# Kernel tuning notes

Hardware: AMD Instinct MI355X
Metric: run time of the kernel (lower is better)

## Reference

```python
import jax, jax.numpy as jnp
import numpy as np

B, T, F, H = 256, 4096, 16, 64

def setup_inputs() -> dict:
    key = jax.random.key(0)
    ks = jax.random.split(key, 16)
    rn = lambda k, s, sc=0.1: jax.random.normal(k, s, dtype=jnp.float32) * sc
    return {
        'x':    rn(ks[0], (B, T, F), 1.0),
        'Wi1':  rn(ks[1], (F, 3 * H)), 'bi1': jnp.zeros((3 * H,), jnp.float32),
        'Whr1': rn(ks[2], (H, H)), 'Whz1': rn(ks[3], (H, H)), 'Whn1': rn(ks[4], (H, H)),
        'bhn1': jnp.zeros((H,), jnp.float32),
        'Wi2':  rn(ks[5], (H, 3 * H)), 'bi2': jnp.zeros((3 * H,), jnp.float32),
        'Whr2': rn(ks[6], (H, H)), 'Whz2': rn(ks[7], (H, H)), 'Whn2': rn(ks[8], (H, H)),
        'bhn2': jnp.zeros((H,), jnp.float32),
        'Wp':   rn(ks[9], (F, H)), 'bp': jnp.zeros((H,), jnp.float32),
        'Wa':   rn(ks[10], (H, 1)), 'ba': jnp.zeros((1,), jnp.float32),
        'W1':   rn(ks[11], (H, 128)), 'b1': jnp.zeros((128,), jnp.float32),
        'W2':   rn(ks[12], (128, 64)), 'b2': jnp.zeros((64,), jnp.float32),
        'W3':   rn(ks[13], (64, 32)), 'b3': jnp.zeros((32,), jnp.float32),
        'W4':   rn(ks[14], (32, 2)), 'b4': jnp.zeros((2,), jnp.float32),
    }

def gru_layer(x, Wi, bi, Whr, Whz, Whn, bhn):
    # flax GRUCell math: r/z hidden kernels bias-free; n hidden kernel has bias.
    b, h = x.shape[0], Whr.shape[0]
    xi = jnp.einsum('btf,fk->btk', x, Wi) + bi  # precompute input projections (B,T,3H)
    def step(hprev, xt):
        ir, iz, inn = jnp.split(xt, 3, axis=-1)
        r = jax.nn.sigmoid(ir + hprev @ Whr)
        z = jax.nn.sigmoid(iz + hprev @ Whz)
        n = jnp.tanh(inn + r * (hprev @ Whn + bhn))
        hnew = (1.0 - z) * n + z * hprev
        return hnew, hnew
    h0 = jnp.zeros((b, h), x.dtype)
    _, ys = jax.lax.scan(step, h0, jnp.swapaxes(xi, 0, 1))  # (T,B,H)
    return jnp.swapaxes(ys, 0, 1)  # (B,T,H)

def reference(x, Wi1, bi1, Whr1, Whz1, Whn1, bhn1,
              Wi2, bi2, Whr2, Whz2, Whn2, bhn2,
              Wp, bp, Wa, ba, W1, b1, W2, b2, W3, b3, W4, b4):
    o1 = gru_layer(x, Wi1, bi1, Whr1, Whz1, Whn1, bhn1)
    x_proj = jnp.einsum('btf,fh->bth', x, Wp) + bp  # F != H -> project
    o1 = o1 + 0.5 * x_proj
    o2 = gru_layer(o1, Wi2, bi2, Whr2, Whz2, Whn2, bhn2) + 0.5 * o1
    scores = jnp.einsum('bth,ho->bto', o2, Wa) + ba  # (B,T,1)
    w = jax.nn.softmax(scores, axis=1)
    attended = jnp.sum(o2 * w, axis=1)  # (B,H)
    h1 = jax.nn.relu(attended @ W1 + b1)
    h2 = jax.nn.relu(h1 @ W2 + b2)
    h3 = jax.nn.relu(h2 @ W3 + b3)
    return h3 @ W4 + b4  # (B,2)
```

## Files before the change

kernel.cpp:

```cpp
#include <hip/hip_runtime.h>


#define B_ 256
#define T_ 4096
#define F_ 16
#define H_ 64
#define L2E 1.4426950408889634f

typedef float v2f __attribute__((ext_vector_type(2)));

__device__ __forceinline__ float sigm(float x) {
    float e = __builtin_amdgcn_exp2f(-L2E * x);
    return __builtin_amdgcn_rcpf(1.0f + e);
}
__device__ __forceinline__ float tanh_(float x) {
    float e = __builtin_amdgcn_exp2f(2.0f * L2E * x);
    return 1.0f - 2.0f * __builtin_amdgcn_rcpf(1.0f + e);
}
__device__ __forceinline__ v2f fma2(v2f a, v2f b, v2f c) {
    return __builtin_elementwise_fma(a, b, c);
}

#define DPPADD(x, ctrl) \
    ((x) + __builtin_bit_cast(float, __builtin_amdgcn_update_dpp( \
        0, __builtin_bit_cast(int, (x)), (ctrl), 0xF, 0xF, true)))

__device__ __forceinline__ float qsum(float x) {
    float t = DPPADD(x, 0xB1);
    return DPPADD(t, 0x4E);
}
__device__ __forceinline__ float wred(float x) {
    x = DPPADD(x, 0x111);
    x = DPPADD(x, 0x112);
    x = DPPADD(x, 0x114);
    x = DPPADD(x, 0x118);
    x = DPPADD(x, 0x142);
    x = DPPADD(x, 0x143);
    return x;
}

__launch_bounds__(512, 1)
__global__ void solar_rnn(const float* __restrict__ x,
                          const float* __restrict__ Wi1, const float* __restrict__ bi1,
                          const float* __restrict__ Whr1, const float* __restrict__ Whz1,
                          const float* __restrict__ Whn1, const float* __restrict__ bhn1,
                          const float* __restrict__ Wi2, const float* __restrict__ bi2,
                          const float* __restrict__ Whr2, const float* __restrict__ Whz2,
                          const float* __restrict__ Whn2, const float* __restrict__ bhn2,
                          const float* __restrict__ Wp, const float* __restrict__ bp,
                          const float* __restrict__ Wa,
                          const float* __restrict__ W1, const float* __restrict__ b1,
                          const float* __restrict__ W2, const float* __restrict__ b2,
                          const float* __restrict__ W3, const float* __restrict__ b3,
                          const float* __restrict__ W4, const float* __restrict__ b4,
                          float* __restrict__ out)
{
    const int b   = blockIdx.x;
    const int tid = threadIdx.x;
    const int w   = tid >> 6;
    const int j   = tid & 63;
    const bool l2r = (w >= 4);
    const int v   = w & 3;
    const int o   = j >> 2;
    const int s   = j & 3;
    const int col = 16 * v + o;

    __shared__ float h1p[2][H_];
    __shared__ float h2p[2][H_];
    __shared__ float o1pl[2][H_];
    __shared__ __align__(16) float xbuf[2][256];
    __shared__ float spl[2][4];
    __shared__ float sm_a[128];
    __shared__ float sm_b[128];

    int hoff[4];
    #pragma unroll
    for (int q = 0; q < 4; ++q) hoff[q] = 16 * s + 4 * ((q + s) & 3);

    v2f hw0[8], hw1[8], hw2[8], hw3[8], hw4[8], hw5[8];
    v2f xw0[2], xw1[2], xw2[2], xw3[2];
    float c0, c1, c2, c3, c4;

    if (!l2r) {
        #pragma unroll
        for (int q = 0; q < 4; ++q) {
            const int rb = hoff[q];
            #pragma unroll
            for (int e = 0; e < 2; ++e) {
                const int r0 = rb + 2 * e, r1 = r0 + 1, m = 2 * q + e;
                hw0[m] = v2f{Whr1[r0 * H_ + col], Whr1[r1 * H_ + col]};
                hw1[m] = v2f{Whz1[r0 * H_ + col], Whz1[r1 * H_ + col]};
                hw2[m] = v2f{Whn1[r0 * H_ + col], Whn1[r1 * H_ + col]};
            }
        }
        #pragma unroll
        for (int m = 0; m < 2; ++m) {
            const int r0 = 4 * s + 2 * m, r1 = r0 + 1;
            xw0[m] = v2f{Wi1[r0 * 192 + col],       Wi1[r1 * 192 + col]};
            xw1[m] = v2f{Wi1[r0 * 192 + 64 + col],  Wi1[r1 * 192 + 64 + col]};
            xw2[m] = v2f{Wi1[r0 * 192 + 128 + col], Wi1[r1 * 192 + 128 + col]};
            xw3[m] = v2f{Wp[r0 * H_ + col],         Wp[r1 * H_ + col]};
        }
        c0 = bi1[col]; c1 = bi1[64 + col]; c2 = bi1[128 + col];
        c3 = bhn1[col]; c4 = bp[col];
    } else {
        #pragma unroll
        for (int q = 0; q < 4; ++q) {
            const int rb = hoff[q];
            #pragma unroll
            for (int e = 0; e < 2; ++e) {
                const int r0 = rb + 2 * e, r1 = r0 + 1, m = 2 * q + e;
                hw0[m] = v2f{Whr2[r0 * H_ + col], Whr2[r1 * H_ + col]};
                hw1[m] = v2f{Whz2[r0 * H_ + col], Whz2[r1 * H_ + col]};
                hw2[m] = v2f{Whn2[r0 * H_ + col], Whn2[r1 * H_ + col]};
                hw3[m] = v2f{Wi2[r0 * 192 + col],       Wi2[r1 * 192 + col]};
                hw4[m] = v2f{Wi2[r0 * 192 + 64 + col],  Wi2[r1 * 192 + 64 + col]};
                hw5[m] = v2f{Wi2[r0 * 192 + 128 + col], Wi2[r1 * 192 + 128 + col]};
            }
        }
        float x2r[4], x2z[4], x2n[4];
        #pragma unroll
        for (int kk = 0; kk < 4; ++kk) {
            const int row = 4 * s + kk;
            float ar = 0.f, az = 0.f, an = 0.f;
            for (int m = 0; m < H_; ++m) {
                const float wp = Wp[row * H_ + m];
                ar = fmaf(wp, Wi2[m * 192 + col],       ar);
                az = fmaf(wp, Wi2[m * 192 + 64 + col],  az);
                an = fmaf(wp, Wi2[m * 192 + 128 + col], an);
            }
            x2r[kk] = 0.5f * ar; x2z[kk] = 0.5f * az; x2n[kk] = 0.5f * an;
        }
        #pragma unroll
        for (int m = 0; m < 2; ++m) {
            xw0[m] = v2f{x2r[2 * m], x2r[2 * m + 1]};
            xw1[m] = v2f{x2z[2 * m], x2z[2 * m + 1]};
            xw2[m] = v2f{x2n[2 * m], x2n[2 * m + 1]};
        }
        float cbr = 0.f, cbz = 0.f, cbn = 0.f;
        for (int m = 0; m < H_; ++m) {
            const float bpm = bp[m];
            cbr = fmaf(bpm, Wi2[m * 192 + col],       cbr);
            cbz = fmaf(bpm, Wi2[m * 192 + 64 + col],  cbz);
            cbn = fmaf(bpm, Wi2[m * 192 + 128 + col], cbn);
        }
        c0 = bi2[col]       + 0.5f * cbr;
        c1 = bi2[64 + col]  + 0.5f * cbz;
        c2 = bi2[128 + col] + 0.5f * cbn;
        c3 = bhn2[col]; c4 = Wa[col];
    }

    if (tid < 64) {
        h1p[0][j] = 0.f; h1p[1][j] = 0.f;
        h2p[0][j] = 0.f; h2p[1][j] = 0.f;
        o1pl[0][j] = 0.f; o1pl[1][j] = 0.f;
    }
    if (tid < 8) spl[tid >> 2][tid & 3] = 0.f;
    const float* xb = x + (size_t)b * T_ * F_;
    float4 xnext;
    if (tid < 64) {
        const float4* gx = (const float4*)xb;
        ((float4*)xbuf[0])[j] = gx[j];
        xnext = gx[64 + j];
    }
    __syncthreads();

    float hS = 0.f;
    float o2a = 0.f;
    float am = -3.0e38f, al = 0.f, aa = 0.f;
    const v2f zz = v2f{0.f, 0.f};

    #pragma unroll 1
    for (int t = 0; t < T_; ++t) {
        const int tb = t & 1;
        if (!l2r) {
            const float4 xt4 = ((const float4*)xbuf[(t >> 4) & 1])[(t & 15) * 4 + s];
            const float* h1r = h1p[tb ^ 1];
            v2f hv[8];
            #pragma unroll
            for (int q = 0; q < 4; ++q) {
                const float4 a = *(const float4*)&h1r[hoff[q]];
                hv[2 * q]     = v2f{a.x, a.y};
                hv[2 * q + 1] = v2f{a.z, a.w};
            }
            const v2f xt0 = v2f{xt4.x, xt4.y}, xt1 = v2f{xt4.z, xt4.w};
            v2f Ar = fma2(xw0[0], xt0, fma2(xw0[1], xt1, zz));
            v2f Az = fma2(xw1[0], xt0, fma2(xw1[1], xt1, zz));
            v2f An = fma2(xw2[0], xt0, fma2(xw2[1], xt1, zz));
            v2f Ax = fma2(xw3[0], xt0, fma2(xw3[1], xt1, zz));
            v2f Ah = zz;
            #pragma unroll
            for (int m = 0; m < 8; ++m) {
                Ar = fma2(hv[m], hw0[m], Ar);
                Az = fma2(hv[m], hw1[m], Az);
                Ah = fma2(hv[m], hw2[m], Ah);
            }
            const float g0 = qsum(Ar.x + Ar.y);
            const float g1 = qsum(Az.x + Az.y);
            const float g2 = qsum(An.x + An.y);
            const float g3 = qsum(Ah.x + Ah.y);
            const float g4 = qsum(Ax.x + Ax.y);
            const float r1 = sigm(g0 + c0);
            const float z1 = sigm(g1 + c1);
            const float n1 = tanh_((g2 + c2) + r1 * (g3 + c3));
            hS = n1 + z1 * (hS - n1);
            const float o1 = hS + 0.5f * (g4 + c4);
            if (s == 0) { h1p[tb][col] = hS; o1pl[tb][col] = o1; }
            if ((t & 15) == 8 && w == 0) {
                const int c = t >> 4;
                if (c + 1 < T_ / 16) {
                    ((float4*)xbuf[(c + 1) & 1])[j] = xnext;
                    if (c + 2 < T_ / 16) xnext = ((const float4*)xb)[(c + 2) * 64 + j];
                }
            }
        } else {
            v2f xm0 = zz, xm1 = zz;
            if (t >= 1) {
                const int tm = t - 1;
                const float4 xm4 = ((const float4*)xbuf[(tm >> 4) & 1])[(tm & 15) * 4 + s];
                xm0 = v2f{xm4.x, xm4.y}; xm1 = v2f{xm4.z, xm4.w};
            }
            const float* h1r = h1p[tb ^ 1];
            const float* h2r = h2p[tb];
            v2f hv[8], gv[8];
            #pragma unroll
            for (int q = 0; q < 4; ++q) {
                const float4 a = *(const float4*)&h1r[hoff[q]];
                const float4 c = *(const float4*)&h2r[hoff[q]];
                hv[2 * q]     = v2f{a.x, a.y};
                hv[2 * q + 1] = v2f{a.z, a.w};
                gv[2 * q]     = v2f{c.x, c.y};
                gv[2 * q + 1] = v2f{c.z, c.w};
            }
            const float o1r = o1pl[tb ^ 1][col];
            float gp = spl[tb][s];

            v2f Ar = fma2(xw0[0], xm0, fma2(xw0[1], xm1, zz));
            v2f Az = fma2(xw1[0], xm0, fma2(xw1[1], xm1, zz));
            v2f An = fma2(xw2[0], xm0, fma2(xw2[1], xm1, zz));
            v2f Ah = zz;
            #pragma unroll
            for (int m = 0; m < 8; ++m) {
                Ar = fma2(gv[m], hw0[m], Ar);
                Az = fma2(gv[m], hw1[m], Az);
                Ah = fma2(gv[m], hw2[m], Ah);
                Ar = fma2(hv[m], hw3[m], Ar);
                Az = fma2(hv[m], hw4[m], Az);
                An = fma2(hv[m], hw5[m], An);
            }
            const float g6 = qsum(Ar.x + Ar.y);
            const float g7 = qsum(Az.x + Az.y);
            const float g5 = qsum(An.x + An.y);
            const float g8 = qsum(Ah.x + Ah.y);
            gp = qsum(gp);

            if (t >= 2) {
                const float p  = 0.25f * gp;
                const float mn = fmaxf(am, p);
                const float ca = __builtin_amdgcn_exp2f((am - mn) * L2E);
                const float ce = __builtin_amdgcn_exp2f((p  - mn) * L2E);
                al = fmaf(al, ca, ce);
                aa = fmaf(aa, ca, ce * o2a);
                am = mn;
            }

            const float r2 = sigm(g6 + c0);
            const float z2 = sigm(g7 + c1);
            const float n2 = tanh_((g5 + c2) + r2 * (g8 + c3));
            hS = n2 + z2 * (hS - n2);
            hS = (t == 0) ? 0.f : hS;
            const float o2 = hS + 0.5f * o1r;
            float ps = wred(o2 * c4);
            if (j == 63) spl[tb ^ 1][v] = ps;
            if (s == 0) h2p[tb ^ 1][col] = hS;
            o2a = o2;
        }
        __syncthreads();
    }

    if (l2r) {
        const int tm = T_ - 1;
        const float4 xm4 = ((const float4*)xbuf[(tm >> 4) & 1])[(tm & 15) * 4 + s];
        const v2f xm0 = v2f{xm4.x, xm4.y}, xm1 = v2f{xm4.z, xm4.w};
        const float* h1r = h1p[1];
        const float* h2r = h2p[0];
        v2f hv[8], gv[8];
        #pragma unroll
        for (int q = 0; q < 4; ++q) {
            const float4 a = *(const float4*)&h1r[hoff[q]];
            const float4 c = *(const float4*)&h2r[hoff[q]];
            hv[2 * q]     = v2f{a.x, a.y};
            hv[2 * q + 1] = v2f{a.z, a.w};
            gv[2 * q]     = v2f{c.x, c.y};
            gv[2 * q + 1] = v2f{c.z, c.w};
        }
        const float o1r = o1pl[1][col];
        v2f Ar = fma2(xw0[0], xm0, fma2(xw0[1], xm1, zz));
        v2f Az = fma2(xw1[0], xm0, fma2(xw1[1], xm1, zz));
        v2f An = fma2(xw2[0], xm0, fma2(xw2[1], xm1, zz));
        v2f Ah = zz;
        #pragma unroll
        for (int m = 0; m < 8; ++m) {
            Ar = fma2(gv[m], hw0[m], Ar);
            Az = fma2(gv[m], hw1[m], Az);
            Ah = fma2(gv[m], hw2[m], Ah);
            Ar = fma2(hv[m], hw3[m], Ar);
            Az = fma2(hv[m], hw4[m], Az);
            An = fma2(hv[m], hw5[m], An);
        }
        const float g6 = qsum(Ar.x + Ar.y);
        const float g7 = qsum(Az.x + Az.y);
        const float g5 = qsum(An.x + An.y);
        const float g8 = qsum(Ah.x + Ah.y);
        float gp = qsum(spl[0][s]);
        {
            const float p  = 0.25f * gp;
            const float mn = fmaxf(am, p);
            const float ca = __builtin_amdgcn_exp2f((am - mn) * L2E);
            const float ce = __builtin_amdgcn_exp2f((p  - mn) * L2E);
            al = fmaf(al, ca, ce);
            aa = fmaf(aa, ca, ce * o2a);
            am = mn;
        }
        const float r2 = sigm(g6 + c0);
        const float z2 = sigm(g7 + c1);
        const float n2 = tanh_((g5 + c2) + r2 * (g8 + c3));
        hS = n2 + z2 * (hS - n2);
        const float o2 = hS + 0.5f * o1r;
        float ps = wred(o2 * c4);
        if (j == 63) spl[1][v] = ps;
        o2a = o2;
    }
    __syncthreads();
    if (l2r) {
        float gq = qsum(spl[1][s]);
        const float p  = 0.25f * gq;
        const float mn = fmaxf(am, p);
        const float ca = __builtin_amdgcn_exp2f((am - mn) * L2E);
        const float ce = __builtin_amdgcn_exp2f((p  - mn) * L2E);
        al = fmaf(al, ca, ce);
        aa = fmaf(aa, ca, ce * o2a);
        if (s == 0) sm_a[col] = aa / al;
    }
    __syncthreads();

    float v1 = 0.f;
    if (tid < 128) {
        float a = b1[tid];
        for (int k = 0; k < 64; ++k) a = fmaf(sm_a[k], W1[k * 128 + tid], a);
        v1 = fmaxf(a, 0.f);
    }
    __syncthreads();
    if (tid < 128) sm_b[tid] = v1;
    __syncthreads();
    if (tid < 64) {
        float a = b2[tid];
        for (int k = 0; k < 128; ++k) a = fmaf(sm_b[k], W2[k * 64 + tid], a);
        sm_a[tid] = fmaxf(a, 0.f);
    }
    __syncthreads();
    if (tid < 32) {
        float a = b3[tid];
        for (int k = 0; k < 64; ++k) a = fmaf(sm_a[k], W3[k * 32 + tid], a);
        sm_b[tid] = fmaxf(a, 0.f);
    }
    __syncthreads();
    if (tid < 2) {
        float a = b4[tid];
        for (int k = 0; k < 32; ++k) a = fmaf(sm_b[k], W4[k * 2 + tid], a);
        out[b * 2 + tid] = a;
    }
}

extern "C" void kernel_launch(void* const* d_in, const int* in_sizes, int n_in,
                              void* d_out, int out_size, void* d_ws, size_t ws_size,
                              hipStream_t stream) {
    const float* x    = (const float*)d_in[0];
    const float* Wi1  = (const float*)d_in[1];
    const float* bi1  = (const float*)d_in[2];
    const float* Whr1 = (const float*)d_in[3];
    const float* Whz1 = (const float*)d_in[4];
    const float* Whn1 = (const float*)d_in[5];
    const float* bhn1 = (const float*)d_in[6];
    const float* Wi2  = (const float*)d_in[7];
    const float* bi2  = (const float*)d_in[8];
    const float* Whr2 = (const float*)d_in[9];
    const float* Whz2 = (const float*)d_in[10];
    const float* Whn2 = (const float*)d_in[11];
    const float* bhn2 = (const float*)d_in[12];
    const float* Wp   = (const float*)d_in[13];
    const float* bp   = (const float*)d_in[14];
    const float* Wa   = (const float*)d_in[15];
    const float* W1   = (const float*)d_in[17];
    const float* b1   = (const float*)d_in[18];
    const float* W2   = (const float*)d_in[19];
    const float* b2   = (const float*)d_in[20];
    const float* W3   = (const float*)d_in[21];
    const float* b3   = (const float*)d_in[22];
    const float* W4   = (const float*)d_in[23];
    const float* b4   = (const float*)d_in[24];

    solar_rnn<<<dim3(B_), dim3(512), 0, stream>>>(
        x, Wi1, bi1, Whr1, Whz1, Whn1, bhn1,
        Wi2, bi2, Whr2, Whz2, Whn2, bhn2,
        Wp, bp, Wa, W1, b1, W2, b2, W3, b3, W4, b4,
        (float*)d_out);
}
```

Before: 2.420 ms.

## Decouple GRU layers with LDS ring buffer and per-wave flag synchronization

Replaces the per-timestep block-wide __syncthreads lockstep between the layer-1 and layer-2 wave groups with a depth-8 LDS ring of layer-1 outputs and per-wave progress counters polled with s_sleep. Layer 2 now consumes the stored o1 (which already includes the input projection) directly, rather than recomputing the x-projection contribution, and layer 1 may run up to a few steps ahead. The goal is to remove barrier stalls on the serial recurrence. The cost is spin-wait polling, and the bounded spin loop breaks after a fixed count, which could silently race if a producer stalls.

```diff
diff --git a/kernel.cpp b/kernel.cpp
--- a/kernel.cpp
+++ b/kernel.cpp
@@ -6,6 +6,7 @@
 #define F_ 16
 #define H_ 64
 #define L2E 1.4426950408889634f
+#define DEPTH 8
 
 typedef float v2f __attribute__((ext_vector_type(2)));
 
@@ -37,6 +38,17 @@
     x = DPPADD(x, 0x142);
     x = DPPADD(x, 0x143);
     return x;
+}
+
+#define LGKM0() asm volatile("s_waitcnt lgkmcnt(0)" ::: "memory")
+
+__device__ __forceinline__ void grpwait(volatile const int* f, int tgt) {
+    int g = 0;
+    while ((f[0] < tgt) | (f[1] < tgt) | (f[2] < tgt) | (f[3] < tgt)) {
+        __builtin_amdgcn_s_sleep(1);
+        if (++g >= 8192) break;
+    }
+    asm volatile("" ::: "memory");
 }
 
 __launch_bounds__(512, 1)
@@ -65,13 +77,16 @@
     const int s   = j & 3;
     const int col = 16 * v + o;
 
-    __shared__ float h1p[2][H_];
-    __shared__ float h2p[2][H_];
-    __shared__ float o1pl[2][H_];
-    __shared__ __align__(16) float xbuf[2][256];
+    __shared__ float h1r[DEPTH][H_];
+    __shared__ float o1g[DEPTH][H_];
+    __shared__ float h2r[2][H_];
     __shared__ float spl[2][4];
+    __shared__ __align__(16) float xsh[2][256];
+    __shared__ int pg1[4], pg2[4];
     __shared__ float sm_a[128];
     __shared__ float sm_b[128];
+    volatile int* vp1 = pg1;
+    volatile int* vp2 = pg2;
 
     int hoff[4];
     #pragma unroll
@@ -118,68 +133,37 @@
                 hw5[m] = v2f{Wi2[r0 * 192 + 128 + col], Wi2[r1 * 192 + 128 + col]};
             }
         }
-        float x2r[4], x2z[4], x2n[4];
-        #pragma unroll
-        for (int kk = 0; kk < 4; ++kk) {
-            const int row = 4 * s + kk;
-            float ar = 0.f, az = 0.f, an = 0.f;
-            for (int m = 0; m < H_; ++m) {
-                const float wp = Wp[row * H_ + m];
-                ar = fmaf(wp, Wi2[m * 192 + col],       ar);
-                az = fmaf(wp, Wi2[m * 192 + 64 + col],  az);
-                an = fmaf(wp, Wi2[m * 192 + 128 + col], an);
-            }
-            x2r[kk] = 0.5f * ar; x2z[kk] = 0.5f * az; x2n[kk] = 0.5f * an;
-        }
-        #pragma unroll
-        for (int m = 0; m < 2; ++m) {
-            xw0[m] = v2f{x2r[2 * m], x2r[2 * m + 1]};
-            xw1[m] = v2f{x2z[2 * m], x2z[2 * m + 1]};
-            xw2[m] = v2f{x2n[2 * m], x2n[2 * m + 1]};
-        }
-        float cbr = 0.f, cbz = 0.f, cbn = 0.f;
-        for (int m = 0; m < H_; ++m) {
-            const float bpm = bp[m];
-            cbr = fmaf(bpm, Wi2[m * 192 + col],       cbr);
-            cbz = fmaf(bpm, Wi2[m * 192 + 64 + col],  cbz);
-            cbn = fmaf(bpm, Wi2[m * 192 + 128 + col], cbn);
-        }
-        c0 = bi2[col]       + 0.5f * cbr;
-        c1 = bi2[64 + col]  + 0.5f * cbz;
-        c2 = bi2[128 + col] + 0.5f * cbn;
+        c0 = bi2[col]; c1 = bi2[64 + col]; c2 = bi2[128 + col];
         c3 = bhn2[col]; c4 = Wa[col];
     }
 
-    if (tid < 64) {
-        h1p[0][j] = 0.f; h1p[1][j] = 0.f;
-        h2p[0][j] = 0.f; h2p[1][j] = 0.f;
-        o1pl[0][j] = 0.f; o1pl[1][j] = 0.f;
-    }
-    if (tid < 8) spl[tid >> 2][tid & 3] = 0.f;
+    if (tid < 64) h1r[DEPTH - 1][j] = 0.f;
+    if (tid < 64) { h2r[0][j] = 0.f; h2r[1][j] = 0.f; }
+    if (tid < 4)  { pg1[tid] = 0; pg2[tid] = 0; }
     const float* xb = x + (size_t)b * T_ * F_;
     float4 xnext;
-    if (tid < 64) {
-        const float4* gx = (const float4*)xb;
-        ((float4*)xbuf[0])[j] = gx[j];
-        xnext = gx[64 + j];
-    }
-    __syncthreads();
-
+    if (w == 0) {
+        ((float4*)&xsh[0][0])[j] = ((const float4*)xb)[j];
+        xnext = ((const float4*)xb)[64 + j];
+    }
+    __syncthreads();
+
+    const v2f zz = v2f{0.f, 0.f};
     float hS = 0.f;
-    float o2a = 0.f;
-    float am = -3.0e38f, al = 0.f, aa = 0.f;
-    const v2f zz = v2f{0.f, 0.f};
-
-    #pragma unroll 1
-    for (int t = 0; t < T_; ++t) {
-        const int tb = t & 1;
-        if (!l2r) {
-            const float4 xt4 = ((const float4*)xbuf[(t >> 4) & 1])[(t & 15) * 4 + s];
-            const float* h1r = h1p[tb ^ 1];
+
+    if (!l2r) {
+        #pragma unroll 1
+        for (int t = 0; t < T_; ++t) {
+            if ((t & 3) == 0 && t >= DEPTH)
+                grpwait(vp2, t - 4);
+            grpwait(vp1, t);
+
+            const float4 xt4 = ((const float4*)xsh[(t >> 4) & 1])[(t & 15) * 4 + s];
+            const float* hr = h1r[(t + DEPTH - 1) & (DEPTH - 1)];
             v2f hv[8];
             #pragma unroll
             for (int q = 0; q < 4; ++q) {
-                const float4 a = *(const float4*)&h1r[hoff[q]];
+                const float4 a = *(const float4*)&hr[hoff[q]];
                 hv[2 * q]     = v2f{a.x, a.y};
                 hv[2 * q + 1] = v2f{a.z, a.w};
             }
@@ -205,48 +189,56 @@
             const float n1 = tanh_((g2 + c2) + r1 * (g3 + c3));
             hS = n1 + z1 * (hS - n1);
             const float o1 = hS + 0.5f * (g4 + c4);
-            if (s == 0) { h1p[tb][col] = hS; o1pl[tb][col] = o1; }
+            if (s == 0) {
+                h1r[t & (DEPTH - 1)][col] = hS;
+                o1g[t & (DEPTH - 1)][col] = o1;
+            }
             if ((t & 15) == 8 && w == 0) {
-                const int c = t >> 4;
-                if (c + 1 < T_ / 16) {
-                    ((float4*)xbuf[(c + 1) & 1])[j] = xnext;
-                    if (c + 2 < T_ / 16) xnext = ((const float4*)xb)[(c + 2) * 64 + j];
+                const int c = (t >> 4) + 1;
+                if (c < T_ / 16) {
+                    ((float4*)&xsh[c & 1][0])[j] = xnext;
+                    if (c + 1 < T_ / 16) xnext = ((const float4*)xb)[(c + 1) * 64 + j];
                 }
             }
-        } else {
-            v2f xm0 = zz, xm1 = zz;
-            if (t >= 1) {
-                const int tm = t - 1;
-                const float4 xm4 = ((const float4*)xbuf[(tm >> 4) & 1])[(tm & 15) * 4 + s];
-                xm0 = v2f{xm4.x, xm4.y}; xm1 = v2f{xm4.z, xm4.w};
-            }
-            const float* h1r = h1p[tb ^ 1];
-            const float* h2r = h2p[tb];
-            v2f hv[8], gv[8];
+            LGKM0();
+            if (j == 0) vp1[v] = t + 1;
+        }
+    } else {
+        float o2a = 0.f;
+        float am = -3.0e38f, al = 0.f, aa = 0.f;
+
+        #pragma unroll 1
+        for (int t = 0; t < T_; ++t) {
+            if ((t & 3) == 0) {
+                const int need = (t + 4 <= T_) ? t + 4 : T_;
+                grpwait(vp1, need);
+            }
+            grpwait(vp2, t);
+
+            const float* orow = o1g[t & (DEPTH - 1)];
+            const float* hr   = h2r[(t + 1) & 1];
+            v2f ov[8], gv[8];
             #pragma unroll
             for (int q = 0; q < 4; ++q) {
-                const float4 a = *(const float4*)&h1r[hoff[q]];
-                const float4 c = *(const float4*)&h2r[hoff[q]];
-                hv[2 * q]     = v2f{a.x, a.y};
-                hv[2 * q + 1] = v2f{a.z, a.w};
+                const float4 a = *(const float4*)&orow[hoff[q]];
+                const float4 c = *(const float4*)&hr[hoff[q]];
+                ov[2 * q]     = v2f{a.x, a.y};
+                ov[2 * q + 1] = v2f{a.z, a.w};
                 gv[2 * q]     = v2f{c.x, c.y};
                 gv[2 * q + 1] = v2f{c.z, c.w};
             }
-            const float o1r = o1pl[tb ^ 1][col];
-            float gp = spl[tb][s];
-
-            v2f Ar = fma2(xw0[0], xm0, fma2(xw0[1], xm1, zz));
-            v2f Az = fma2(xw1[0], xm0, fma2(xw1[1], xm1, zz));
-            v2f An = fma2(xw2[0], xm0, fma2(xw2[1], xm1, zz));
-            v2f Ah = zz;
+            const float o1own = orow[col];
+            float gp = spl[(t + 1) & 1][s];
+
+            v2f Ar = zz, Az = zz, An = zz, Ah = zz;
             #pragma unroll
             for (int m = 0; m < 8; ++m) {
+                Ar = fma2(ov[m], hw3[m], Ar);
+                Az = fma2(ov[m], hw4[m], Az);
+                An = fma2(ov[m], hw5[m], An);
                 Ar = fma2(gv[m], hw0[m], Ar);
                 Az = fma2(gv[m], hw1[m], Az);
                 Ah = fma2(gv[m], hw2[m], Ah);
-                Ar = fma2(hv[m], hw3[m], Ar);
-                Az = fma2(hv[m], hw4[m], Az);
-                An = fma2(hv[m], hw5[m], An);
             }
             const float g6 = qsum(Ar.x + Ar.y);
             const float g7 = qsum(Az.x + Az.y);
@@ -254,7 +246,7 @@
             const float g8 = qsum(Ah.x + Ah.y);
             gp = qsum(gp);
 
-            if (t >= 2) {
+            if (t >= 1) {
                 const float p  = 0.25f * gp;
                 const float mn = fmaxf(am, p);
                 const float ca = __builtin_amdgcn_exp2f((am - mn) * L2E);
@@ -268,80 +260,27 @@
             const float z2 = sigm(g7 + c1);
             const float n2 = tanh_((g5 + c2) + r2 * (g8 + c3));
             hS = n2 + z2 * (hS - n2);
-            hS = (t == 0) ? 0.f : hS;
-            const float o2 = hS + 0.5f * o1r;
+            const float o2 = hS + 0.5f * o1own;
             float ps = wred(o2 * c4);
-            if (j == 63) spl[tb ^ 1][v] = ps;
-            if (s == 0) h2p[tb ^ 1][col] = hS;
+            if (j == 63) spl[t & 1][v] = ps;
+            if (s == 0) h2r[t & 1][col] = hS;
             o2a = o2;
-        }
-        __syncthreads();
-    }
-
-    if (l2r) {
-        const int tm = T_ - 1;
-        const float4 xm4 = ((const float4*)xbuf[(tm >> 4) & 1])[(tm & 15) * 4 + s];
-        const v2f xm0 = v2f{xm4.x, xm4.y}, xm1 = v2f{xm4.z, xm4.w};
-        const float* h1r = h1p[1];
-        const float* h2r = h2p[0];
-        v2f hv[8], gv[8];
-        #pragma unroll
-        for (int q = 0; q < 4; ++q) {
-            const float4 a = *(const float4*)&h1r[hoff[q]];
-            const float4 c = *(const float4*)&h2r[hoff[q]];
-            hv[2 * q]     = v2f{a.x, a.y};
-            hv[2 * q + 1] = v2f{a.z, a.w};
-            gv[2 * q]     = v2f{c.x, c.y};
-            gv[2 * q + 1] = v2f{c.z, c.w};
-        }
-        const float o1r = o1pl[1][col];
-        v2f Ar = fma2(xw0[0], xm0, fma2(xw0[1], xm1, zz));
-        v2f Az = fma2(xw1[0], xm0, fma2(xw1[1], xm1, zz));
-        v2f An = fma2(xw2[0], xm0, fma2(xw2[1], xm1, zz));
-        v2f Ah = zz;
-        #pragma unroll
-        for (int m = 0; m < 8; ++m) {
-            Ar = fma2(gv[m], hw0[m], Ar);
-            Az = fma2(gv[m], hw1[m], Az);
-            Ah = fma2(gv[m], hw2[m], Ah);
-            Ar = fma2(hv[m], hw3[m], Ar);
-            Az = fma2(hv[m], hw4[m], Az);
-            An = fma2(hv[m], hw5[m], An);
-        }
-        const float g6 = qsum(Ar.x + Ar.y);
-        const float g7 = qsum(Az.x + Az.y);
-        const float g5 = qsum(An.x + An.y);
-        const float g8 = qsum(Ah.x + Ah.y);
-        float gp = qsum(spl[0][s]);
+            LGKM0();
+            if (j == 0) vp2[v] = t + 1;
+        }
+        grpwait(vp2, T_);
+        float gq = qsum(spl[(T_ + 1) & 1][s]);
         {
-            const float p  = 0.25f * gp;
+            const float p  = 0.25f * gq;
             const float mn = fmaxf(am, p);
             const float ca = __builtin_amdgcn_exp2f((am - mn) * L2E);
             const float ce = __builtin_amdgcn_exp2f((p  - mn) * L2E);
             al = fmaf(al, ca, ce);
             aa = fmaf(aa, ca, ce * o2a);
-            am = mn;
-        }
-        const float r2 = sigm(g6 + c0);
-        const float z2 = sigm(g7 + c1);
-        const float n2 = tanh_((g5 + c2) + r2 * (g8 + c3));
-        hS = n2 + z2 * (hS - n2);
-        const float o2 = hS + 0.5f * o1r;
-        float ps = wred(o2 * c4);
-        if (j == 63) spl[1][v] = ps;
-        o2a = o2;
-    }
-    __syncthreads();
-    if (l2r) {
-        float gq = qsum(spl[1][s]);
-        const float p  = 0.25f * gq;
-        const float mn = fmaxf(am, p);
-        const float ca = __builtin_amdgcn_exp2f((am - mn) * L2E);
-        const float ce = __builtin_amdgcn_exp2f((p  - mn) * L2E);
-        al = fmaf(al, ca, ce);
-        aa = fmaf(aa, ca, ce * o2a);
+        }
         if (s == 0) sm_a[col] = aa / al;
     }
+
     __syncthreads();
 
     float v1 = 0.f;
```

Measured after the change: 3.157 ms. 1.3x slower.
